# Kernel tuning notes

Hardware: AMD Instinct MI355X
Metric: run time of the kernel (lower is better)

Reference implementation:

```python
import jax, jax.numpy as jnp
import numpy as np

S, B, NC, IMG = 7, 2, 20, 448
GRID = IMG // S  # 64 px per cell
COORD_W, NOOBJ_W = 5.0, 0.5
N_BATCH, N_GT = 16384, 20


def _left_top():
    # ltp[i, j] = (GRID * j, GRID * i)  -- x from column, y from row
    col = (jnp.arange(S) * GRID).astype(jnp.float32)
    X, Y = jnp.meshgrid(col, col, indexing='xy')
    return jnp.stack([X, Y], -1)  # [S, S, 2]


def _corners(center_xy, wh):
    half = wh * 0.5
    x1y1 = jnp.clip(center_xy - half, 0.0, IMG - 1.0)
    x2y2 = jnp.clip(center_xy + half, 0.0, IMG - 1.0)
    return jnp.concatenate([x1y1, x2y2], -1)


def _encode(groundTruth, groundLabels):
    # Vectorized objMaskAndEncoder: replaces nested python scatter loops.
    N, G, _ = groundTruth.shape
    x1, y1, x2, y2 = (groundTruth[..., k] for k in range(4))
    w, h = x2 - x1, y2 - y1
    x, y = x1 + w * 0.5, y1 + h * 0.5
    cellX = jnp.floor(x / GRID).astype(jnp.int32)
    cellY = jnp.floor(y / GRID).astype(jnp.int32)
    offset = jnp.stack([(x - cellX * GRID) / GRID,
                        (y - cellY * GRID) / GRID,
                        w / IMG, h / IMG], -1)  # [N, G, 4]
    b_idx = jnp.broadcast_to(jnp.arange(N)[:, None], (N, G))
    flat = cellY * S + cellX  # [N, G] flat cell id
    j_idx = jnp.broadcast_to(jnp.arange(G, dtype=jnp.int32)[None, :], (N, G))
    last = jnp.full((N, S * S), -1, jnp.int32).at[b_idx, flat].max(j_idx)
    gi = jnp.maximum(last, 0)
    gathered = jnp.take_along_axis(offset, gi[:, :, None], axis=1)  # [N, S*S, 4]
    gtOrd = jnp.where((last >= 0)[:, :, None], gathered, 0.0).reshape(N, S, S, 4)
    # every GT sets its class bit in its cell (not just the last one)
    gtLabels = jnp.zeros((N, S, S, NC), jnp.float32).at[
        b_idx, cellY, cellX, groundLabels].set(1.0)
    objMask = (gtLabels.sum(-1) != 0).astype(jnp.float32)
    return objMask, gtOrd, gtLabels


def _best_iou(objMask, gtOrd, preBoxes):
    N = preBoxes.shape[0]
    ltp = _left_top()
    pb = preBoxes.reshape(N, S, S, B, 4)
    pboxes = _corners(pb[..., :2] * GRID + ltp[None, :, :, None, :],
                      pb[..., 2:] * IMG)  # [N, S, S, B, 4]
    gboxes = _corners(gtOrd[..., :2] * GRID + ltp[None, :, :, :],
                      gtOrd[..., 2:] * IMG)[:, :, :, None, :]  # [N, S, S, 1, 4]
    lt = jnp.maximum(pboxes[..., :2], gboxes[..., :2])
    rb = jnp.minimum(pboxes[..., 2:], gboxes[..., 2:])
    wh = jnp.maximum(rb - lt, 0.0)
    inter = wh[..., 0] * wh[..., 1]
    a1 = (pboxes[..., 2] - pboxes[..., 0]) * (pboxes[..., 3] - pboxes[..., 1])
    a2 = (gboxes[..., 2] - gboxes[..., 0]) * (gboxes[..., 3] - gboxes[..., 1])
    iou = inter / (a1 + a2 - inter + 1e-4)  # [N, S, S, B]
    best = jnp.argmax(iou, axis=-1)
    boxObjMask = jax.nn.one_hot(best, B, dtype=jnp.float32) * objMask[..., None]
    boxIouMax = jnp.max(iou, axis=-1, keepdims=True) * boxObjMask
    return boxObjMask, boxIouMax


def _yolo_loss(preConfidence, preBoxes, preCondClasses, groundTruth, groundLabels):
    objMask, gtOrd, gtLabels = _encode(groundTruth, groundLabels)
    boxObjMask, _ = _best_iou(objMask, gtOrd, preBoxes)
    objMask, gtOrd, gtLabels, boxObjMask = map(
        jax.lax.stop_gradient, (objMask, gtOrd, gtLabels, boxObjMask))  # torch no_grad
    pb = preBoxes.reshape(-1, S, S, B, 4)
    m = boxObjMask[..., None]
    xy, wh = pb[..., :2], jnp.sqrt(pb[..., 2:])
    xyGt = gtOrd[..., None, :2]
    whGt = jnp.sqrt(gtOrd[..., None, 2:])
    coordLoss = ((jnp.square(xy - xyGt) * m).sum()
                 + (jnp.square(wh - whGt) * m).sum()) * COORD_W
    diff2 = jnp.square(preConfidence - boxObjMask)
    objLoss = (diff2 * boxObjMask).sum()
    noObjLoss = NOOBJ_W * (diff2 * (1.0 - boxObjMask)).sum()
    clsLoss = (jnp.square(preCondClasses - gtLabels).sum(-1) * objMask).sum()
    return coordLoss, objLoss, noObjLoss, clsLoss


def setup_inputs() -> dict:
    key = jax.random.key(0)
    k1, k2, k3, k4, k5, k6 = jax.random.split(key, 6)
    preConfidence = jax.random.uniform(k1, (N_BATCH, S, S, B), jnp.float32)
    preBoxes = jax.random.uniform(k2, (N_BATCH, S, S, B * 4), jnp.float32)
    preCondClasses = jax.random.uniform(k3, (N_BATCH, S, S, NC), jnp.float32)
    # realistic GT corner boxes inside the 448x448 image
    cxy = jax.random.uniform(k4, (N_BATCH, N_GT, 2), jnp.float32, 0.0, float(IMG))
    wh = jax.random.uniform(k5, (N_BATCH, N_GT, 2), jnp.float32, 10.0, 120.0)
    x1y1 = jnp.clip(cxy - wh / 2, 0.0, IMG - 1.0)
    x2y2 = jnp.clip(cxy + wh / 2, 0.0, IMG - 1.0)
    groundTruth = jnp.concatenate([x1y1, x2y2], -1)
    groundLabels = jax.random.randint(k6, (N_BATCH, N_GT), 0, NC)
    return {"preConfidence": preConfidence, "preBoxes": preBoxes,
            "preCondClasses": preCondClasses, "groundTruth": groundTruth,
            "groundLabels": groundLabels}


def reference(preConfidence, preBoxes, preCondClasses, groundTruth, groundLabels):
    return _yolo_loss(preConfidence, preBoxes, preCondClasses, groundTruth, groundLabels)
```

## Files before the change

kernel.cpp:

```cpp
#include <hip/hip_runtime.h>
#include <math.h>


#define S7 7
#define NCELL 49
#define NGT 20
#define NCLS 20
#define BPB 4
#define BPW 2
#define THREADS 256
#define NBLK 2048

__device__ __forceinline__ float clip447(float v) {
    return fminf(fmaxf(v, 0.0f), 447.0f);
}

__device__ __forceinline__ float iou_one(float4 pb, float ltx, float lty,
                                         float g1x, float g1y, float g2x, float g2y,
                                         float ga) {
    float cx = pb.x * 64.0f + ltx, cy = pb.y * 64.0f + lty;
    float w  = pb.z * 448.0f,      h  = pb.w * 448.0f;
    float p1x = clip447(cx - w * 0.5f), p1y = clip447(cy - h * 0.5f);
    float p2x = clip447(cx + w * 0.5f), p2y = clip447(cy + h * 0.5f);
    float lx = fmaxf(p1x, g1x), ly = fmaxf(p1y, g1y);
    float rx = fminf(p2x, g2x), ry = fminf(p2y, g2y);
    float iw = fmaxf(rx - lx, 0.0f), ih = fmaxf(ry - ly, 0.0f);
    float inter = iw * ih;
    float a1 = (p2x - p1x) * (p2y - p1y);
    return inter / (a1 + ga - inter + 0.0001f);
}

__global__ __launch_bounds__(THREADS) void yolo_loss_kernel(
    const float* __restrict__ preConf,
    const float* __restrict__ preBoxes,
    const float* __restrict__ preCls,
    const float* __restrict__ gtBox,
    const int*   __restrict__ gtLab,
    float* __restrict__ ws)
{
    __shared__ float s_red[BPB][4];

    const int wave = threadIdx.x >> 6;
    const int lane = threadIdx.x & 63;

    float coordL = 0.0f, objL = 0.0f, noobjL = 0.0f, clsL = 0.0f;

    for (int it = 0; it < BPW; ++it) {
        const int n = it * (NBLK * BPB) + blockIdx.x * BPB + wave;

        float offx = 0.f, offy = 0.f, offw = 0.f, offh = 0.f;
        int flatv = 0, lab = 0;
        if (lane < NGT) {
            float4 g = reinterpret_cast<const float4*>(gtBox)[(size_t)n * NGT + lane];
            lab = gtLab[(size_t)n * NGT + lane];
            float w = g.z - g.x, h = g.w - g.y;
            float x = g.x + 0.5f * w, y = g.y + 0.5f * h;
            int cx = (int)floorf(x * 0.015625f);
            int cy = (int)floorf(y * 0.015625f);
            flatv = cy * S7 + cx;
            offx = (x - (float)cx * 64.0f) * 0.015625f;
            offy = (y - (float)cy * 64.0f) * 0.015625f;
            offw = w * (1.0f / 448.0f);
            offh = h * (1.0f / 448.0f);
        }

        int last = -1;
        unsigned bits = 0u;
        #pragma unroll
        for (int j = 0; j < NGT; ++j) {
            int fj = __shfl(flatv, j);
            int lj = __shfl(lab, j);
            if (fj == lane) { last = j; bits |= (1u << lj); }
        }
        const unsigned long long ball = __ballot(bits != 0u);

        const int srcl = (last < 0) ? 0 : last;
        const float gx = __shfl(offx, srcl);
        const float gy = __shfl(offy, srcl);
        const float gw = __shfl(offw, srcl);
        const float gh = __shfl(offh, srcl);

        if (lane < NCELL) {
            const int row = lane / S7, col = lane - row * S7;
            const float ltx = (float)col * 64.0f, lty = (float)row * 64.0f;

            float2 cf = reinterpret_cast<const float2*>(preConf)[(size_t)n * NCELL + lane];
            if (last >= 0) {
                const float4* pbp = reinterpret_cast<const float4*>(preBoxes)
                                    + (size_t)n * NCELL * 2 + (size_t)lane * 2;
                float4 b0 = pbp[0];
                float4 b1 = pbp[1];

                float gcx = gx * 64.0f + ltx, gcy = gy * 64.0f + lty;
                float gW = gw * 448.0f, gH = gh * 448.0f;
                float g1x = clip447(gcx - gW * 0.5f), g1y = clip447(gcy - gH * 0.5f);
                float g2x = clip447(gcx + gW * 0.5f), g2y = clip447(gcy + gH * 0.5f);
                float ga = (g2x - g1x) * (g2y - g1y);

                float iou0 = iou_one(b0, ltx, lty, g1x, g1y, g2x, g2y, ga);
                float iou1 = iou_one(b1, ltx, lty, g1x, g1y, g2x, g2y, ga);
                int best = (iou1 > iou0) ? 1 : 0;
                float4 pb = best ? b1 : b0;
                float confB = best ? cf.y : cf.x;
                float confO = best ? cf.x : cf.y;

                float dx = pb.x - gx, dy = pb.y - gy;
                float dw = sqrtf(pb.z) - sqrtf(gw);
                float dh = sqrtf(pb.w) - sqrtf(gh);
                coordL += dx * dx + dy * dy + dw * dw + dh * dh;
                float d = confB - 1.0f;
                objL += d * d;
                noobjL += confO * confO;
            } else {
                noobjL += cf.x * cf.x + cf.y * cf.y;
            }
        }

        {
            const float4* base4 = reinterpret_cast<const float4*>(
                preCls + (size_t)n * (NCELL * NCLS));
            #pragma unroll
            for (int t = 0; t < 4; ++t) {
                const int i = lane + t * 64;
                if (i < 245) {
                    const int c0 = i / 5;
                    const int k0 = (i - c0 * 5) * 4;
                    if ((ball >> c0) & 1ull) {
                        const unsigned b = __shfl(bits, c0);
                        float4 v = base4[i];
                        float d0 = v.x - (float)((b >> (k0 + 0)) & 1u);
                        float d1 = v.y - (float)((b >> (k0 + 1)) & 1u);
                        float d2 = v.z - (float)((b >> (k0 + 2)) & 1u);
                        float d3 = v.w - (float)((b >> (k0 + 3)) & 1u);
                        clsL += d0 * d0 + d1 * d1 + d2 * d2 + d3 * d3;
                    }
                }
            }
        }
    }

    for (int off = 32; off > 0; off >>= 1) {
        coordL += __shfl_down(coordL, off);
        objL   += __shfl_down(objL, off);
        noobjL += __shfl_down(noobjL, off);
        clsL   += __shfl_down(clsL, off);
    }
    if (lane == 0) {
        s_red[wave][0] = coordL;
        s_red[wave][1] = objL;
        s_red[wave][2] = noobjL;
        s_red[wave][3] = clsL;
    }
    __syncthreads();

    if (threadIdx.x == 0) {
        float c0 = 0.f, c1 = 0.f, c2 = 0.f, c3 = 0.f;
        for (int w = 0; w < BPB; ++w) {
            c0 += s_red[w][0];
            c1 += s_red[w][1];
            c2 += s_red[w][2];
            c3 += s_red[w][3];
        }
        ws[0 * NBLK + blockIdx.x] = c0 * 5.0f;
        ws[1 * NBLK + blockIdx.x] = c1;
        ws[2 * NBLK + blockIdx.x] = c2 * 0.5f;
        ws[3 * NBLK + blockIdx.x] = c3;
    }
}

__global__ __launch_bounds__(256) void reduce_kernel(
    const float* __restrict__ ws, float* __restrict__ out)
{
    const int wave = threadIdx.x >> 6;
    const int lane = threadIdx.x & 63;
    const float* src = ws + wave * NBLK;
    float s = 0.0f;
    for (int i = lane; i < NBLK; i += 64) s += src[i];
    for (int off = 32; off > 0; off >>= 1) s += __shfl_down(s, off);
    if (lane == 0) out[wave] = s;
}

extern "C" void kernel_launch(void* const* d_in, const int* in_sizes, int n_in,
                              void* d_out, int out_size, void* d_ws, size_t ws_size,
                              hipStream_t stream) {
    const float* preConf  = (const float*)d_in[0];
    const float* preBoxes = (const float*)d_in[1];
    const float* preCls   = (const float*)d_in[2];
    const float* gtBox    = (const float*)d_in[3];
    const int*   gtLab    = (const int*)d_in[4];
    float* out = (float*)d_out;
    float* ws  = (float*)d_ws;

    yolo_loss_kernel<<<NBLK, THREADS, 0, stream>>>(
        preConf, preBoxes, preCls, gtBox, gtLab, ws);
    reduce_kernel<<<1, 256, 0, stream>>>(ws, out);
}
```

Baseline: 142.0 us.

## Interleave two samples per wave to overlap their global loads

The two-iteration per-wave loop is manually unrolled so both samples' GT boxes, labels, confidences, boxes and class rows are loaded up front, with the second sample's class loads issued before the first sample's class math. Cell index and label are also packed into one int so the per-GT match loop needs one shuffle per sample instead of two. The goal is more memory-level parallelism in a latency-bound kernel. The cost is higher register pressure from the doubled live state, which may reduce occupancy.

```diff
diff --git a/kernel.cpp b/kernel.cpp
--- a/kernel.cpp
+++ b/kernel.cpp
@@ -7,7 +7,6 @@
 #define NGT 20
 #define NCLS 20
 #define BPB 4
-#define BPW 2
 #define THREADS 256
 #define NBLK 2048
 
@@ -42,100 +41,189 @@
 
     const int wave = threadIdx.x >> 6;
     const int lane = threadIdx.x & 63;
-
-    float coordL = 0.0f, objL = 0.0f, noobjL = 0.0f, clsL = 0.0f;
-
-    for (int it = 0; it < BPW; ++it) {
-        const int n = it * (NBLK * BPB) + blockIdx.x * BPB + wave;
-
-        float offx = 0.f, offy = 0.f, offw = 0.f, offh = 0.f;
-        int flatv = 0, lab = 0;
-        if (lane < NGT) {
-            float4 g = reinterpret_cast<const float4*>(gtBox)[(size_t)n * NGT + lane];
-            lab = gtLab[(size_t)n * NGT + lane];
-            float w = g.z - g.x, h = g.w - g.y;
-            float x = g.x + 0.5f * w, y = g.y + 0.5f * h;
+    const int n0 = blockIdx.x * BPB + wave;
+    const int n1 = n0 + NBLK * BPB;
+
+    float4 g0, g1;
+    int pk0 = 0, pk1 = 0;
+    if (lane < NGT) {
+        g0 = reinterpret_cast<const float4*>(gtBox)[(size_t)n0 * NGT + lane];
+        g1 = reinterpret_cast<const float4*>(gtBox)[(size_t)n1 * NGT + lane];
+        pk0 = gtLab[(size_t)n0 * NGT + lane] << 8;
+        pk1 = gtLab[(size_t)n1 * NGT + lane] << 8;
+    }
+    float2 cf0, cf1;
+    if (lane < NCELL) {
+        cf0 = reinterpret_cast<const float2*>(preConf)[(size_t)n0 * NCELL + lane];
+        cf1 = reinterpret_cast<const float2*>(preConf)[(size_t)n1 * NCELL + lane];
+    }
+
+    float ox0 = 0, oy0 = 0, ow0 = 0, oh0 = 0;
+    float ox1 = 0, oy1 = 0, ow1 = 0, oh1 = 0;
+    if (lane < NGT) {
+        {
+            float w = g0.z - g0.x, h = g0.w - g0.y;
+            float x = g0.x + 0.5f * w, y = g0.y + 0.5f * h;
             int cx = (int)floorf(x * 0.015625f);
             int cy = (int)floorf(y * 0.015625f);
-            flatv = cy * S7 + cx;
-            offx = (x - (float)cx * 64.0f) * 0.015625f;
-            offy = (y - (float)cy * 64.0f) * 0.015625f;
-            offw = w * (1.0f / 448.0f);
-            offh = h * (1.0f / 448.0f);
-        }
-
-        int last = -1;
-        unsigned bits = 0u;
+            pk0 |= cy * S7 + cx;
+            ox0 = (x - (float)cx * 64.0f) * 0.015625f;
+            oy0 = (y - (float)cy * 64.0f) * 0.015625f;
+            ow0 = w * (1.0f / 448.0f);
+            oh0 = h * (1.0f / 448.0f);
+        }
+        {
+            float w = g1.z - g1.x, h = g1.w - g1.y;
+            float x = g1.x + 0.5f * w, y = g1.y + 0.5f * h;
+            int cx = (int)floorf(x * 0.015625f);
+            int cy = (int)floorf(y * 0.015625f);
+            pk1 |= cy * S7 + cx;
+            ox1 = (x - (float)cx * 64.0f) * 0.015625f;
+            oy1 = (y - (float)cy * 64.0f) * 0.015625f;
+            ow1 = w * (1.0f / 448.0f);
+            oh1 = h * (1.0f / 448.0f);
+        }
+    }
+
+    int last0 = -1, last1 = -1;
+    unsigned bits0 = 0u, bits1 = 0u;
+    #pragma unroll
+    for (int j = 0; j < NGT; ++j) {
+        int p0 = __shfl(pk0, j);
+        int p1 = __shfl(pk1, j);
+        if ((p0 & 63) == lane) { last0 = j; bits0 |= (1u << (p0 >> 8)); }
+        if ((p1 & 63) == lane) { last1 = j; bits1 |= (1u << (p1 >> 8)); }
+    }
+    const unsigned long long ball0 = __ballot(bits0 != 0u);
+    const unsigned long long ball1 = __ballot(bits1 != 0u);
+
+    const int s0 = (last0 < 0) ? 0 : last0;
+    const int s1 = (last1 < 0) ? 0 : last1;
+    const float gx0 = __shfl(ox0, s0), gy0 = __shfl(oy0, s0);
+    const float gw0 = __shfl(ow0, s0), gh0 = __shfl(oh0, s0);
+    const float gx1 = __shfl(ox1, s1), gy1 = __shfl(oy1, s1);
+    const float gw1 = __shfl(ow1, s1), gh1 = __shfl(oh1, s1);
+
+    const bool obj0 = (lane < NCELL) && (last0 >= 0);
+    const bool obj1 = (lane < NCELL) && (last1 >= 0);
+    float4 b00, b01, b10, b11;
+    if (obj0) {
+        const float4* p = reinterpret_cast<const float4*>(preBoxes)
+                          + (size_t)n0 * NCELL * 2 + (size_t)lane * 2;
+        b00 = p[0]; b01 = p[1];
+    }
+    if (obj1) {
+        const float4* p = reinterpret_cast<const float4*>(preBoxes)
+                          + (size_t)n1 * NCELL * 2 + (size_t)lane * 2;
+        b10 = p[0]; b11 = p[1];
+    }
+
+    float4 cv0[4];
+    bool   cp0[4];
+    {
+        const float4* base4 = reinterpret_cast<const float4*>(
+            preCls + (size_t)n0 * (NCELL * NCLS));
         #pragma unroll
-        for (int j = 0; j < NGT; ++j) {
-            int fj = __shfl(flatv, j);
-            int lj = __shfl(lab, j);
-            if (fj == lane) { last = j; bits |= (1u << lj); }
-        }
-        const unsigned long long ball = __ballot(bits != 0u);
-
-        const int srcl = (last < 0) ? 0 : last;
-        const float gx = __shfl(offx, srcl);
-        const float gy = __shfl(offy, srcl);
-        const float gw = __shfl(offw, srcl);
-        const float gh = __shfl(offh, srcl);
-
-        if (lane < NCELL) {
-            const int row = lane / S7, col = lane - row * S7;
-            const float ltx = (float)col * 64.0f, lty = (float)row * 64.0f;
-
-            float2 cf = reinterpret_cast<const float2*>(preConf)[(size_t)n * NCELL + lane];
-            if (last >= 0) {
-                const float4* pbp = reinterpret_cast<const float4*>(preBoxes)
-                                    + (size_t)n * NCELL * 2 + (size_t)lane * 2;
-                float4 b0 = pbp[0];
-                float4 b1 = pbp[1];
-
-                float gcx = gx * 64.0f + ltx, gcy = gy * 64.0f + lty;
-                float gW = gw * 448.0f, gH = gh * 448.0f;
-                float g1x = clip447(gcx - gW * 0.5f), g1y = clip447(gcy - gH * 0.5f);
-                float g2x = clip447(gcx + gW * 0.5f), g2y = clip447(gcy + gH * 0.5f);
-                float ga = (g2x - g1x) * (g2y - g1y);
-
-                float iou0 = iou_one(b0, ltx, lty, g1x, g1y, g2x, g2y, ga);
-                float iou1 = iou_one(b1, ltx, lty, g1x, g1y, g2x, g2y, ga);
-                int best = (iou1 > iou0) ? 1 : 0;
-                float4 pb = best ? b1 : b0;
-                float confB = best ? cf.y : cf.x;
-                float confO = best ? cf.x : cf.y;
-
-                float dx = pb.x - gx, dy = pb.y - gy;
-                float dw = sqrtf(pb.z) - sqrtf(gw);
-                float dh = sqrtf(pb.w) - sqrtf(gh);
-                coordL += dx * dx + dy * dy + dw * dw + dh * dh;
-                float d = confB - 1.0f;
-                objL += d * d;
-                noobjL += confO * confO;
-            } else {
-                noobjL += cf.x * cf.x + cf.y * cf.y;
-            }
-        }
-
-        {
-            const float4* base4 = reinterpret_cast<const float4*>(
-                preCls + (size_t)n * (NCELL * NCLS));
-            #pragma unroll
-            for (int t = 0; t < 4; ++t) {
-                const int i = lane + t * 64;
-                if (i < 245) {
-                    const int c0 = i / 5;
-                    const int k0 = (i - c0 * 5) * 4;
-                    if ((ball >> c0) & 1ull) {
-                        const unsigned b = __shfl(bits, c0);
-                        float4 v = base4[i];
-                        float d0 = v.x - (float)((b >> (k0 + 0)) & 1u);
-                        float d1 = v.y - (float)((b >> (k0 + 1)) & 1u);
-                        float d2 = v.z - (float)((b >> (k0 + 2)) & 1u);
-                        float d3 = v.w - (float)((b >> (k0 + 3)) & 1u);
-                        clsL += d0 * d0 + d1 * d1 + d2 * d2 + d3 * d3;
-                    }
-                }
-            }
+        for (int t = 0; t < 4; ++t) {
+            const int i = lane + t * 64;
+            const int c = i / 5;
+            cp0[t] = (i < 245) && ((ball0 >> c) & 1ull);
+            if (cp0[t]) cv0[t] = base4[i];
+        }
+    }
+
+    float coordL = 0.0f, objL = 0.0f, noobjL = 0.0f, clsL = 0.0f;
+
+    const int row = lane / S7, col = lane - row * S7;
+    const float ltx = (float)col * 64.0f, lty = (float)row * 64.0f;
+
+    if (lane < NCELL) {
+        if (obj0) {
+            float gcx = gx0 * 64.0f + ltx, gcy = gy0 * 64.0f + lty;
+            float gW = gw0 * 448.0f, gH = gh0 * 448.0f;
+            float g1x = clip447(gcx - gW * 0.5f), g1y = clip447(gcy - gH * 0.5f);
+            float g2x = clip447(gcx + gW * 0.5f), g2y = clip447(gcy + gH * 0.5f);
+            float ga = (g2x - g1x) * (g2y - g1y);
+            float iou0 = iou_one(b00, ltx, lty, g1x, g1y, g2x, g2y, ga);
+            float iou1 = iou_one(b01, ltx, lty, g1x, g1y, g2x, g2y, ga);
+            int best = (iou1 > iou0) ? 1 : 0;
+            float4 pb = best ? b01 : b00;
+            float confB = best ? cf0.y : cf0.x;
+            float confO = best ? cf0.x : cf0.y;
+            float dx = pb.x - gx0, dy = pb.y - gy0;
+            float dw = sqrtf(pb.z) - sqrtf(gw0);
+            float dh = sqrtf(pb.w) - sqrtf(gh0);
+            coordL += dx * dx + dy * dy + dw * dw + dh * dh;
+            float d = confB - 1.0f;
+            objL += d * d;
+            noobjL += confO * confO;
+        } else {
+            noobjL += cf0.x * cf0.x + cf0.y * cf0.y;
+        }
+        if (obj1) {
+            float gcx = gx1 * 64.0f + ltx, gcy = gy1 * 64.0f + lty;
+            float gW = gw1 * 448.0f, gH = gh1 * 448.0f;
+            float g1x = clip447(gcx - gW * 0.5f), g1y = clip447(gcy - gH * 0.5f);
+            float g2x = clip447(gcx + gW * 0.5f), g2y = clip447(gcy + gH * 0.5f);
+            float ga = (g2x - g1x) * (g2y - g1y);
+            float iou0 = iou_one(b10, ltx, lty, g1x, g1y, g2x, g2y, ga);
+            float iou1 = iou_one(b11, ltx, lty, g1x, g1y, g2x, g2y, ga);
+            int best = (iou1 > iou0) ? 1 : 0;
+            float4 pb = best ? b11 : b10;
+            float confB = best ? cf1.y : cf1.x;
+            float confO = best ? cf1.x : cf1.y;
+            float dx = pb.x - gx1, dy = pb.y - gy1;
+            float dw = sqrtf(pb.z) - sqrtf(gw1);
+            float dh = sqrtf(pb.w) - sqrtf(gh1);
+            coordL += dx * dx + dy * dy + dw * dw + dh * dh;
+            float d = confB - 1.0f;
+            objL += d * d;
+            noobjL += confO * confO;
+        } else {
+            noobjL += cf1.x * cf1.x + cf1.y * cf1.y;
+        }
+    }
+
+    float4 cv1[4];
+    bool   cp1[4];
+    {
+        const float4* base4 = reinterpret_cast<const float4*>(
+            preCls + (size_t)n1 * (NCELL * NCLS));
+        #pragma unroll
+        for (int t = 0; t < 4; ++t) {
+            const int i = lane + t * 64;
+            const int c = i / 5;
+            cp1[t] = (i < 245) && ((ball1 >> c) & 1ull);
+            if (cp1[t]) cv1[t] = base4[i];
+        }
+    }
+
+    #pragma unroll
+    for (int t = 0; t < 4; ++t) {
+        if (cp0[t]) {
+            const int i = lane + t * 64;
+            const int c = i / 5;
+            const int k0 = (i - c * 5) * 4;
+            const unsigned b = __shfl(bits0, c);
+            float d0 = cv0[t].x - (float)((b >> (k0 + 0)) & 1u);
+            float d1 = cv0[t].y - (float)((b >> (k0 + 1)) & 1u);
+            float d2 = cv0[t].z - (float)((b >> (k0 + 2)) & 1u);
+            float d3 = cv0[t].w - (float)((b >> (k0 + 3)) & 1u);
+            clsL += d0 * d0 + d1 * d1 + d2 * d2 + d3 * d3;
+        }
+    }
+    #pragma unroll
+    for (int t = 0; t < 4; ++t) {
+        if (cp1[t]) {
+            const int i = lane + t * 64;
+            const int c = i / 5;
+            const int k0 = (i - c * 5) * 4;
+            const unsigned b = __shfl(bits1, c);
+            float d0 = cv1[t].x - (float)((b >> (k0 + 0)) & 1u);
+            float d1 = cv1[t].y - (float)((b >> (k0 + 1)) & 1u);
+            float d2 = cv1[t].z - (float)((b >> (k0 + 2)) & 1u);
+            float d3 = cv1[t].w - (float)((b >> (k0 + 3)) & 1u);
+            clsL += d0 * d0 + d1 * d1 + d2 * d2 + d3 * d3;
         }
     }
 
```

Result: faster. 135.6 us (-4.5%).
